# Kernel optimization log

Hardware: AMD Instinct MI355X
Metric: run time of the kernel (lower is better)

Reference implementation:

```python
import jax, jax.numpy as jnp
import numpy as np

S = 4096  # source_sequence_size
Q = 4096  # query_sequence_size
E = 2048  # embedding_size
D = 2048  # output_embedding_size


def setup_inputs() -> dict:
    key = jax.random.key(0)
    ks = jax.random.split(key, 9)
    s = 1.0 / np.sqrt(E)
    return {
        "key": jax.random.normal(ks[0], (S, E), jnp.float32),
        "value": jax.random.normal(ks[1], (S, E), jnp.float32),
        "query": jax.random.normal(ks[2], (Q, E), jnp.float32),
        "Wk": jax.random.normal(ks[3], (D, E), jnp.float32) * s,
        "bk": jax.random.normal(ks[4], (D,), jnp.float32) * 0.01,
        "Wq": jax.random.normal(ks[5], (D, E), jnp.float32) * s,
        "bq": jax.random.normal(ks[6], (D,), jnp.float32) * 0.01,
        "Wv": jax.random.normal(ks[7], (D, E), jnp.float32) * s,
        "bv": jax.random.normal(ks[8], (D,), jnp.float32) * 0.01,
    }


def reference(key, value, query, Wk, bk, Wq, bq, Wv, bv):
    # Linear projections (nn.Linear: x @ W.T + b)
    k = key @ Wk.T + bk      # [S, D]
    v = value @ Wv.T + bv    # [S, D]
    q = query @ Wq.T + bq    # [Q, D]
    # Per-query-token attention scores over all source tokens (schema BOTH),
    # then weighted sum over value rows -- vectorized form of the per-token
    # apply_attention_scores loop.
    scale = 1.0 / jnp.sqrt(jnp.asarray(D, q.dtype))
    scores = jax.nn.softmax(jnp.einsum("qd,sd->qs", q, k) * scale, axis=-1)  # [Q, S]
    return jnp.einsum("qs,sd->qd", scores, v)  # [Q, D]
```

## Files before the change

kernel.cpp:

```cpp
#include <hip/hip_runtime.h>

#define S_SEQ 4096
#define Q_SEQ 4096
#define E_DIM 2048
#define D_DIM 2048

typedef __bf16 bf16;
typedef __bf16 bf16x4 __attribute__((ext_vector_type(4)));
typedef __bf16 bf16x8 __attribute__((ext_vector_type(8)));
typedef float f32x4 __attribute__((ext_vector_type(4)));

__global__ __launch_bounds__(256) void cast6(
    const float* __restrict__ i0, const float* __restrict__ i1,
    const float* __restrict__ i2, const float* __restrict__ i3,
    const float* __restrict__ i4, const float* __restrict__ i5,
    bf16* __restrict__ o0, bf16* __restrict__ o1, bf16* __restrict__ o2,
    bf16* __restrict__ o3, bf16* __restrict__ o4, bf16* __restrict__ o5) {
  const float* in;
  bf16* out;
  int n4;
  switch (blockIdx.y) {
    case 0: in = i0; out = o0; n4 = (S_SEQ * E_DIM) / 4; break;
    case 1: in = i1; out = o1; n4 = (S_SEQ * E_DIM) / 4; break;
    case 2: in = i2; out = o2; n4 = (S_SEQ * E_DIM) / 4; break;
    case 3: in = i3; out = o3; n4 = (D_DIM * E_DIM) / 4; break;
    case 4: in = i4; out = o4; n4 = (D_DIM * E_DIM) / 4; break;
    default: in = i5; out = o5; n4 = (D_DIM * E_DIM) / 4; break;
  }
  int i = blockIdx.x * 256 + threadIdx.x;
  if (i < n4) {
    float4 v = reinterpret_cast<const float4*>(in)[i];
    bf16x4 o;
    o[0] = (bf16)v.x; o[1] = (bf16)v.y; o[2] = (bf16)v.z; o[3] = (bf16)v.w;
    *reinterpret_cast<bf16x4*>(out + 4 * (size_t)i) = o;
  }
}

__device__ __forceinline__ void async_copy16(const bf16* g, bf16* l) {
  __builtin_amdgcn_global_load_lds(
      (const __attribute__((address_space(1))) void*)g,
      (__attribute__((address_space(3))) void*)l, 16, 0, 0);
}

__device__ __forceinline__ void xcd_remap(int id, int nt, int& m, int& n) {
  int xcd = id & 7;
  int lid = id >> 3;
  m = (xcd & 3) * 4 + (lid & 3);
  n = (xcd >> 2) * (nt >> 1) + (lid >> 2);
}

__device__ __forceinline__ void stage_half(const bf16* __restrict__ G, int ld,
                                           int grow0, int k0, bf16* lds,
                                           int wave, int lane) {
#pragma unroll
  for (int s = 0; s < 2; ++s) {
    int c = (wave * 2 + s) * 64 + lane;
    int row = c >> 3;
    int kc = (c & 7) ^ (row & 7);
    const bf16* g = G + (size_t)(grow0 + row) * ld + k0 + kc * 8;
    async_copy16(g, lds + (size_t)(wave * 2 + s) * 512);
  }
}

#define BARRIER __builtin_amdgcn_s_barrier()
#define LGKM0 asm volatile("s_waitcnt lgkmcnt(0)" ::: "memory")
#define VMCNT2 asm volatile("s_waitcnt vmcnt(2)" ::: "memory")
#define VMCNT0 asm volatile("s_waitcnt vmcnt(0)" ::: "memory")

#define RD_A(buf, IP)                                                         \
  _Pragma("unroll") for (int ii = 0; ii < 2; ++ii)                            \
  _Pragma("unroll") for (int kk = 0; kk < 2; ++kk)                            \
      aR[ii][kk] = *(const bf16x8*)(&Als[buf][(size_t)(wRow + ((IP)*2 + ii) * 16 + lrow) * 64 + slotk[kk] * 8]);

#define RD_B(buf, JP, dst)                                                    \
  _Pragma("unroll") for (int jj = 0; jj < 2; ++jj)                            \
  _Pragma("unroll") for (int kk = 0; kk < 2; ++kk)                            \
      dst[jj][kk] = *(const bf16x8*)(&Bls[buf][(size_t)(wCol + ((JP)*2 + jj) * 16 + lrow) * 64 + slotk[kk] * 8]);

#define MMA16(IP)                                                              \
  __builtin_amdgcn_s_setprio(1);                                               \
  _Pragma("unroll") for (int jj = 0; jj < 2; ++jj)                             \
  _Pragma("unroll") for (int ii = 0; ii < 2; ++ii)                             \
  _Pragma("unroll") for (int kk = 0; kk < 2; ++kk)                             \
      acc[(IP)*2 + ii][jj] = __builtin_amdgcn_mfma_f32_16x16x32_bf16(          \
          aR[ii][kk], b0[jj][kk], acc[(IP)*2 + ii][jj], 0, 0, 0);              \
  _Pragma("unroll") for (int jj = 0; jj < 2; ++jj)                             \
  _Pragma("unroll") for (int ii = 0; ii < 2; ++ii)                             \
  _Pragma("unroll") for (int kk = 0; kk < 2; ++kk)                             \
      acc[(IP)*2 + ii][2 + jj] = __builtin_amdgcn_mfma_f32_16x16x32_bf16(      \
          aR[ii][kk], b1[jj][kk], acc[(IP)*2 + ii][2 + jj], 0, 0, 0);          \
  __builtin_amdgcn_s_setprio(0)

template <int EPI>
__device__ __forceinline__ void gemm_body(
    const bf16* __restrict__ A, int lda,
    const bf16* __restrict__ B, int ldb,
    void* __restrict__ C, int ldc,
    const float* __restrict__ aux, float scale, int K, int mBase, int nBase) {
  __shared__ __align__(16) bf16 Als[2][256 * 64];
  __shared__ __align__(16) bf16 Bls[2][128 * 64];

  const int tid  = threadIdx.x;
  const int wave = tid >> 6;
  const int lane = tid & 63;
  const int quad = lane >> 4;
  const int lrow = lane & 15;
  const int wRow = (wave >> 1) * 64;
  const int wCol = (wave & 1) * 64;
  const int slotk[2] = {quad ^ (lrow & 7), (4 + quad) ^ (lrow & 7)};

  f32x4 acc[4][4];
#pragma unroll
  for (int i = 0; i < 4; ++i)
#pragma unroll
    for (int j = 0; j < 4; ++j) {
      f32x4 z = {0.f, 0.f, 0.f, 0.f};
      acc[i][j] = z;
    }

  bf16x8 aR[2][2], b0[2][2], b1[2][2];

  stage_half(B, ldb, nBase, 0, &Bls[0][0], wave, lane);
  stage_half(A, lda, mBase, 0, &Als[0][0], wave, lane);
  stage_half(A, lda, mBase + 128, 0, &Als[0][128 * 64], wave, lane);
  stage_half(B, ldb, nBase, 64, &Bls[1][0], wave, lane);
  VMCNT2;
  BARRIER;

  const int NI = K >> 7;
#pragma unroll 1
  for (int i = 0; i < NI; ++i) {
    const bool nl = (i + 1 < NI);
    const int kb = i * 128;
    RD_A(0, 0);
    RD_B(0, 0, b0);
    RD_B(0, 1, b1);
    stage_half(A, lda, mBase, kb + 64, &Als[1][0], wave, lane);
    stage_half(A, lda, mBase + 128, kb + 64, &Als[1][128 * 64], wave, lane);
    BARRIER; LGKM0; MMA16(0); BARRIER;
    RD_A(0, 1);
    if (nl) {
      stage_half(B, ldb, nBase, kb + 128, &Bls[0][0], wave, lane);
      VMCNT2;
    } else {
      VMCNT0;
    }
    BARRIER; LGKM0; MMA16(1); BARRIER;
    RD_A(1, 0);
    RD_B(1, 0, b0);
    RD_B(1, 1, b1);
    if (nl) {
      stage_half(A, lda, mBase, kb + 128, &Als[0][0], wave, lane);
      stage_half(A, lda, mBase + 128, kb + 128, &Als[0][128 * 64], wave, lane);
    }
    BARRIER; LGKM0; MMA16(0); BARRIER;
    RD_A(1, 1);
    if (nl) {
      stage_half(B, ldb, nBase, kb + 192, &Bls[1][0], wave, lane);
      VMCNT2;
    }
    BARRIER; LGKM0; MMA16(1); BARRIER;
  }

  float rinv[4][4];
  if (EPI == 2) {
#pragma unroll
    for (int i = 0; i < 4; ++i)
#pragma unroll
      for (int r = 0; r < 4; ++r)
        rinv[i][r] = aux[mBase + wRow + i * 16 + quad * 4 + r];
  }
#pragma unroll
  for (int j = 0; j < 4; ++j) {
    const int cn = nBase + wCol + j * 16 + lrow;
    float bj = 0.f;
    if (EPI == 0) bj = aux[cn];
#pragma unroll
    for (int i = 0; i < 4; ++i) {
      const int rbase = mBase + wRow + i * 16 + quad * 4;
#pragma unroll
      for (int r = 0; r < 4; ++r) {
        if (EPI == 0)
          ((bf16*)C)[(size_t)(rbase + r) * ldc + cn] = (bf16)(acc[i][j][r] + bj);
        else if (EPI == 1)
          ((bf16*)C)[(size_t)(rbase + r) * ldc + cn] =
              (bf16)__expf(acc[i][j][r] * scale);
        else
          ((float*)C)[(size_t)(rbase + r) * ldc + cn] = acc[i][j][r] * rinv[i][r];
      }
    }
  }
}

__global__ __launch_bounds__(512, 2) void qk_gemm(
    const bf16* __restrict__ A, const bf16* __restrict__ B,
    bf16* __restrict__ E, float scale) {
  int m, n;
  xcd_remap(blockIdx.x, 32, m, n);
  gemm_body<1>(A, D_DIM, B, D_DIM, (void*)E, S_SEQ, nullptr, scale, D_DIM,
               m * 256, n * 128);
}

__global__ __launch_bounds__(512, 2) void pv_gemm(
    const bf16* __restrict__ E, const bf16* __restrict__ vT,
    float* __restrict__ out, const float* __restrict__ inv) {
  int m, n;
  xcd_remap(blockIdx.x, 16, m, n);
  gemm_body<2>(E, S_SEQ, vT, S_SEQ, (void*)out, D_DIM, inv, 0.f, S_SEQ,
               m * 256, n * 128);
}

__global__ __launch_bounds__(512, 2) void proj_gemm(
    const bf16* __restrict__ xk, const bf16* __restrict__ xq,
    const bf16* __restrict__ xv,
    const bf16* __restrict__ Wk, const bf16* __restrict__ Wq,
    const bf16* __restrict__ Wv,
    const float* __restrict__ bk, const float* __restrict__ bq,
    const float* __restrict__ bv,
    bf16* __restrict__ ok, bf16* __restrict__ oq, bf16* __restrict__ ov) {
  const bf16 *A, *W;
  const float* b;
  bf16* o;
  switch (blockIdx.z) {
    case 0: A = xk; W = Wk; b = bk; o = ok; break;
    case 1: A = xq; W = Wq; b = bq; o = oq; break;
    default: A = xv; W = Wv; b = bv; o = ov; break;
  }
  int m, n;
  xcd_remap(blockIdx.x, 16, m, n);
  gemm_body<0>(A, E_DIM, W, E_DIM, (void*)o, D_DIM, b, 0.f, E_DIM,
               m * 256, n * 128);
}

__global__ __launch_bounds__(256) void transpose_bf16(
    const bf16* __restrict__ in, bf16* __restrict__ out) {
  __shared__ bf16 tile[64][66];
  const int t = threadIdx.x;
  const int c0 = blockIdx.x * 64;
  const int r0 = blockIdx.y * 64;
  const int col = t & 63;
  const int r4 = t >> 6;
#pragma unroll
  for (int i = 0; i < 16; ++i) {
    int rr = i * 4 + r4;
    tile[rr][col] = in[(size_t)(r0 + rr) * D_DIM + c0 + col];
  }
  __syncthreads();
#pragma unroll
  for (int i = 0; i < 16; ++i) {
    int rr = i * 4 + r4;
    out[(size_t)(c0 + rr) * S_SEQ + r0 + col] = tile[col][rr];
  }
}

__global__ __launch_bounds__(256) void rowsum_inv(
    const bf16* __restrict__ E, float* __restrict__ inv) {
  const int t = threadIdx.x;
  const int wave = t >> 6;
  const int lane = t & 63;
  const int row = blockIdx.x * 4 + wave;
  const bf16x8* src = (const bf16x8*)(E + (size_t)row * S_SEQ);
  float s = 0.f;
#pragma unroll
  for (int i = 0; i < 8; ++i) {
    bf16x8 v = src[lane + i * 64];
#pragma unroll
    for (int j = 0; j < 8; ++j) s += (float)v[j];
  }
#pragma unroll
  for (int off = 32; off > 0; off >>= 1)
    s += __shfl_down(s, off, 64);
  if (lane == 0) inv[row] = 1.0f / s;
}

extern "C" void kernel_launch(void* const* d_in, const int* in_sizes, int n_in,
                              void* d_out, int out_size, void* d_ws, size_t ws_size,
                              hipStream_t stream) {
  const float* key   = (const float*)d_in[0];
  const float* value = (const float*)d_in[1];
  const float* query = (const float*)d_in[2];
  const float* Wk = (const float*)d_in[3];
  const float* bk = (const float*)d_in[4];
  const float* Wq = (const float*)d_in[5];
  const float* bq = (const float*)d_in[6];
  const float* Wv = (const float*)d_in[7];
  const float* bv = (const float*)d_in[8];

  const size_t MB = 1ull << 20;
  char* ws = (char*)d_ws;
  bf16* key_bf   = (bf16*)(ws + 0 * MB);
  bf16* value_bf = (bf16*)(ws + 16 * MB);
  bf16* query_bf = (bf16*)(ws + 32 * MB);
  bf16* Wk_bf    = (bf16*)(ws + 48 * MB);
  bf16* Wq_bf    = (bf16*)(ws + 56 * MB);
  bf16* Wv_bf    = (bf16*)(ws + 64 * MB);
  bf16* k_bf     = (bf16*)(ws + 72 * MB);
  bf16* q_bf     = (bf16*)(ws + 88 * MB);
  bf16* v_bf     = (bf16*)(ws + 104 * MB);
  bf16* vT_bf    = (bf16*)(ws + 120 * MB);
  bf16* E        = (bf16*)(ws + 0 * MB);
  float* inv     = (float*)(ws + 34 * MB);

  dim3 blk(256);
  dim3 blk512(512);

  cast6<<<dim3(8192, 6), blk, 0, stream>>>(
      key, value, query, Wk, Wq, Wv,
      key_bf, value_bf, query_bf, Wk_bf, Wq_bf, Wv_bf);

  proj_gemm<<<dim3(256, 1, 3), blk512, 0, stream>>>(
      key_bf, query_bf, value_bf, Wk_bf, Wq_bf, Wv_bf, bk, bq, bv,
      k_bf, q_bf, v_bf);

  transpose_bf16<<<dim3(D_DIM / 64, S_SEQ / 64), blk, 0, stream>>>(v_bf, vT_bf);

  const float scale = 0.022097086912079608f;
  qk_gemm<<<dim3(512), blk512, 0, stream>>>(q_bf, k_bf, E, scale);

  rowsum_inv<<<dim3(1024), blk, 0, stream>>>(E, inv);

  pv_gemm<<<dim3(256), blk512, 0, stream>>>(E, vT_bf, (float*)d_out, inv);
}
```

Measured before the change: 423.7 us.

## Use single-buffered 128x128 tile GEMM for projection kernels

The projection GEMM moves from the double-buffered 256x128 four-phase body with 512 threads to a new simple single-buffered 128x128 body with 256 threads. The grid doubles to 512 blocks per projection, with a matching XCD remap over 32 row tiles. The aim is better occupancy and load balance across CUs for the three projections. The cost is that single buffering leaves global loads unoverlapped with MFMA work, and smaller tiles mean less data reuse.

```diff
diff --git a/kernel.cpp b/kernel.cpp
--- a/kernel.cpp
+++ b/kernel.cpp
@@ -42,11 +42,116 @@
       (__attribute__((address_space(3))) void*)l, 16, 0, 0);
 }
 
-__device__ __forceinline__ void xcd_remap(int id, int nt, int& m, int& n) {
+__device__ __forceinline__ void xcd_remap32(int id, int nt, int& m, int& n) {
+  int xcd = id & 7;
+  int lid = id >> 3;
+  m = (xcd & 3) * 8 + (lid & 7);
+  n = (xcd >> 2) * (nt >> 1) + (lid >> 3);
+}
+__device__ __forceinline__ void xcd_remap16(int id, int nt, int& m, int& n) {
   int xcd = id & 7;
   int lid = id >> 3;
   m = (xcd & 3) * 4 + (lid & 3);
   n = (xcd >> 2) * (nt >> 1) + (lid >> 2);
+}
+
+template <int EPI>
+__device__ __forceinline__ void gemm_body_sb(
+    const bf16* __restrict__ A, int lda,
+    const bf16* __restrict__ B, int ldb,
+    void* __restrict__ C, int ldc,
+    const float* __restrict__ aux, float scale, int K, int mBase, int nBase) {
+  __shared__ __align__(16) bf16 Als[128 * 64];
+  __shared__ __align__(16) bf16 Bls[128 * 64];
+
+  const int tid  = threadIdx.x;
+  const int wave = tid >> 6;
+  const int lane = tid & 63;
+  const int quad = lane >> 4;
+  const int lrow = lane & 15;
+  const int wRow = (wave >> 1) * 64;
+  const int wCol = (wave & 1) * 64;
+
+  f32x4 acc[4][4];
+#pragma unroll
+  for (int i = 0; i < 4; ++i)
+#pragma unroll
+    for (int j = 0; j < 4; ++j) {
+      f32x4 z = {0.f, 0.f, 0.f, 0.f};
+      acc[i][j] = z;
+    }
+
+  for (int k0 = 0; k0 < K; k0 += 64) {
+#pragma unroll
+    for (int c = 0; c < 4; ++c) {
+      int chunk = c * 256 + tid;
+      int row = chunk >> 3;
+      int kc = (chunk & 7) ^ (row & 7);
+      const bf16* g = A + (size_t)(mBase + row) * lda + k0 + kc * 8;
+      async_copy16(g, Als + (size_t)(c * 256 + wave * 64) * 8);
+    }
+#pragma unroll
+    for (int c = 0; c < 4; ++c) {
+      int chunk = c * 256 + tid;
+      int row = chunk >> 3;
+      int kc = (chunk & 7) ^ (row & 7);
+      const bf16* g = B + (size_t)(nBase + row) * ldb + k0 + kc * 8;
+      async_copy16(g, Bls + (size_t)(c * 256 + wave * 64) * 8);
+    }
+    __syncthreads();
+
+#pragma unroll
+    for (int kk = 0; kk < 2; ++kk) {
+      bf16x8 af[4], bfr[4];
+#pragma unroll
+      for (int i = 0; i < 4; ++i) {
+        int r = wRow + i * 16 + lrow;
+        int slot = (kk * 4 + quad) ^ (r & 7);
+        af[i] = *(const bf16x8*)(Als + (size_t)r * 64 + slot * 8);
+      }
+#pragma unroll
+      for (int j = 0; j < 4; ++j) {
+        int r = wCol + j * 16 + lrow;
+        int slot = (kk * 4 + quad) ^ (r & 7);
+        bfr[j] = *(const bf16x8*)(Bls + (size_t)r * 64 + slot * 8);
+      }
+#pragma unroll
+      for (int i = 0; i < 4; ++i)
+#pragma unroll
+        for (int j = 0; j < 4; ++j)
+          acc[i][j] = __builtin_amdgcn_mfma_f32_16x16x32_bf16(af[i], bfr[j], acc[i][j], 0, 0, 0);
+    }
+    __syncthreads();
+  }
+
+  float rinv[4][4];
+  if (EPI == 2) {
+#pragma unroll
+    for (int i = 0; i < 4; ++i)
+#pragma unroll
+      for (int r = 0; r < 4; ++r)
+        rinv[i][r] = aux[mBase + wRow + i * 16 + quad * 4 + r];
+  }
+#pragma unroll
+  for (int j = 0; j < 4; ++j) {
+    const int cn = nBase + wCol + j * 16 + lrow;
+    float bj = 0.f;
+    if (EPI == 0) bj = aux[cn];
+#pragma unroll
+    for (int i = 0; i < 4; ++i) {
+      const int rbase = mBase + wRow + i * 16 + quad * 4;
+#pragma unroll
+      for (int r = 0; r < 4; ++r) {
+        if (EPI == 0)
+          ((bf16*)C)[(size_t)(rbase + r) * ldc + cn] = (bf16)(acc[i][j][r] + bj);
+        else if (EPI == 1)
+          ((bf16*)C)[(size_t)(rbase + r) * ldc + cn] =
+              (bf16)__expf(acc[i][j][r] * scale);
+        else
+          ((float*)C)[(size_t)(rbase + r) * ldc + cn] = acc[i][j][r] * rinv[i][r];
+      }
+    }
+  }
 }
 
 __device__ __forceinline__ void stage_half(const bf16* __restrict__ G, int ld,
@@ -92,7 +197,7 @@
   __builtin_amdgcn_s_setprio(0)
 
 template <int EPI>
-__device__ __forceinline__ void gemm_body(
+__device__ __forceinline__ void gemm_body_4ph(
     const bf16* __restrict__ A, int lda,
     const bf16* __restrict__ B, int ldb,
     void* __restrict__ C, int ldc,
@@ -196,21 +301,21 @@
     const bf16* __restrict__ A, const bf16* __restrict__ B,
     bf16* __restrict__ E, float scale) {
   int m, n;
-  xcd_remap(blockIdx.x, 32, m, n);
-  gemm_body<1>(A, D_DIM, B, D_DIM, (void*)E, S_SEQ, nullptr, scale, D_DIM,
-               m * 256, n * 128);
+  xcd_remap16(blockIdx.x, 32, m, n);
+  gemm_body_4ph<1>(A, D_DIM, B, D_DIM, (void*)E, S_SEQ, nullptr, scale, D_DIM,
+                   m * 256, n * 128);
 }
 
 __global__ __launch_bounds__(512, 2) void pv_gemm(
     const bf16* __restrict__ E, const bf16* __restrict__ vT,
     float* __restrict__ out, const float* __restrict__ inv) {
   int m, n;
-  xcd_remap(blockIdx.x, 16, m, n);
-  gemm_body<2>(E, S_SEQ, vT, S_SEQ, (void*)out, D_DIM, inv, 0.f, S_SEQ,
-               m * 256, n * 128);
-}
-
-__global__ __launch_bounds__(512, 2) void proj_gemm(
+  xcd_remap16(blockIdx.x, 16, m, n);
+  gemm_body_4ph<2>(E, S_SEQ, vT, S_SEQ, (void*)out, D_DIM, inv, 0.f, S_SEQ,
+                   m * 256, n * 128);
+}
+
+__global__ __launch_bounds__(256, 2) void proj_gemm(
     const bf16* __restrict__ xk, const bf16* __restrict__ xq,
     const bf16* __restrict__ xv,
     const bf16* __restrict__ Wk, const bf16* __restrict__ Wq,
@@ -227,9 +332,9 @@
     default: A = xv; W = Wv; b = bv; o = ov; break;
   }
   int m, n;
-  xcd_remap(blockIdx.x, 16, m, n);
-  gemm_body<0>(A, E_DIM, W, E_DIM, (void*)o, D_DIM, b, 0.f, E_DIM,
-               m * 256, n * 128);
+  xcd_remap32(blockIdx.x, 16, m, n);
+  gemm_body_sb<0>(A, E_DIM, W, E_DIM, (void*)o, D_DIM, b, 0.f, E_DIM,
+                  m * 128, n * 128);
 }
 
 __global__ __launch_bounds__(256) void transpose_bf16(
@@ -308,7 +413,7 @@
       key, value, query, Wk, Wq, Wv,
       key_bf, value_bf, query_bf, Wk_bf, Wq_bf, Wv_bf);
 
-  proj_gemm<<<dim3(256, 1, 3), blk512, 0, stream>>>(
+  proj_gemm<<<dim3(512, 1, 3), blk, 0, stream>>>(
       key_bf, query_bf, value_bf, Wk_bf, Wq_bf, Wv_bf, bk, bq, bv,
       k_bf, q_bf, v_bf);
 
```

New measurement: 416.0 us. Within noise of the previous version (-1.8%).
